# Performance work log

Measured on AMD Instinct MI355X. Metric: run time of the kernel, lower is better.

Reference implementation:

```python
import jax, jax.numpy as jnp
import numpy as np

EPS = 1e-8

def setup_inputs() -> dict:
    key = jax.random.key(0)
    k1, k2, k3, k4 = jax.random.split(key, 4)
    b, in_c, out_c, style_c, k, h, w = 8, 512, 512, 512, 3, 64, 64
    return {
        "input": jax.random.normal(k1, (b, in_c, h, w), dtype=jnp.float32),
        "style": jax.random.normal(k2, (b, style_c), dtype=jnp.float32),
        "w_affine": jax.random.normal(k3, (in_c, style_c), dtype=jnp.float32),  # Linear weight, init N(0,1), runtime-scaled
        "b_affine": jnp.ones((1, in_c), dtype=jnp.float32),                     # Bias init_value=1.0
        "w_conv": jax.random.normal(k4, (out_c, in_c, k, k), dtype=jnp.float32),
    }

def reference(input, style, w_affine, b_affine, w_conv):
    b, in_c, h, w = input.shape
    out_c, _, kh, kw = w_conv.shape
    # Equalized-LR runtime scales (lr_mul=1):
    affine_scale = 1.0 / (w_affine.shape[1] ** 0.5)          # he_std for Linear
    conv_scale = 1.0 / ((in_c * kh * kw) ** 0.5)             # he_std for conv weight
    # affine: Linear + Bias (bias initialized to 1.0)
    s = style @ w_affine.T * affine_scale + b_affine          # [b, in_c]
    # modulate: per-sample weight tensor [b, out_c, in_c, kh, kw]
    wgt = s[:, None, :, None, None] * (w_conv * conv_scale)[None]
    # demodulate
    demod = jax.lax.rsqrt(jnp.sum(wgt * wgt, axis=(2, 3, 4), keepdims=True) + EPS)
    wgt = wgt * demod
    # grouped conv with groups = batch (stride=1, padding=1)
    x = input.reshape(1, b * in_c, h, w)
    wgt = wgt.reshape(b * out_c, in_c, kh, kw)
    out = jax.lax.conv_general_dilated(
        x, wgt,
        window_strides=(1, 1),
        padding=[(1, 1), (1, 1)],
        dimension_numbers=("NCHW", "OIHW", "NCHW"),
        feature_group_count=b,
    )
    return out.reshape(b, out_c, h, w)
```

## Files before the change

### kernel.cpp

```cpp
#include <hip/hip_runtime.h>
#include <hip/hip_bf16.h>

#define BB 8
#define CIN 512
#define COUT 512
#define HH 64
#define WW 64

#define AFF_SCALE 0.044194173824159216f
#define CONV_SCALE 0.014731391274719736f
#define CONV_SCALE2 (1.0f/4608.0f)

typedef short s16x8 __attribute__((ext_vector_type(8)));
typedef float f32x16 __attribute__((ext_vector_type(16)));

__device__ __forceinline__ unsigned short f2bf(float f) {
  __hip_bfloat16 h = __float2bfloat16(f);
  return *reinterpret_cast<unsigned short*>(&h);
}

__device__ __forceinline__ void gload_lds16(const void* g, void* l) {
  __builtin_amdgcn_global_load_lds(
      (const __attribute__((address_space(1))) unsigned int*)g,
      (__attribute__((address_space(3))) unsigned int*)l, 16, 0, 0);
}

__global__ __launch_bounds__(256) void prep1_kernel(
    const float* __restrict__ style, const float* __restrict__ wa,
    const float* __restrict__ ba, float* __restrict__ smod,
    const float* __restrict__ wc, float* __restrict__ wsq,
    ushort* __restrict__ wfrag) {
  int bb = blockIdx.x;
  if (bb < 1024) {
    int wid  = (bb << 2) + (threadIdx.x >> 6);
    int lane = threadIdx.x & 63;
    int b  = wid >> 9;
    int ic = wid & 511;
    const float* s = style + b * CIN;
    const float* w = wa + (size_t)ic * CIN;
    float sum = 0.f;
#pragma unroll
    for (int k = 0; k < CIN / 64; ++k) sum += s[lane + 64 * k] * w[lane + 64 * k];
#pragma unroll
    for (int off = 32; off; off >>= 1) sum += __shfl_down(sum, off, 64);
    if (lane == 0) smod[wid] = sum * AFF_SCALE + ba[ic];
  } else if (bb < 2048) {
    int i = (bb - 1024) * 256 + threadIdx.x;
    const float* p = wc + (size_t)i * 9;
    float s = 0.f;
#pragma unroll
    for (int k = 0; k < 9; ++k) { float v = p[k]; s += v * v; }
    wsq[i] = s;
  } else {
    int n = (bb - 2048) * 256 + threadIdx.x;
    int l    = n & 63;
    int ks   = (n >> 6) & 1;
    int mf   = (n >> 7) & 15;
    int widx = n >> 11;
    int g = widx / 9, p = widx % 9;
    int kh = p % 3, kw = p / 3;
    int oc  = mf * 32 + (l & 31);
    int ic0 = g * 32 + ks * 16 + 8 * (l >> 5);
    s16x8 o;
#pragma unroll
    for (int j = 0; j < 8; ++j) {
      float v = wc[((size_t)oc * CIN + ic0 + j) * 9 + kh * 3 + kw];
      o[j] = (short)f2bf(v);
    }
    *(s16x8*)(wfrag + (size_t)n * 8) = o;
  }
}

__global__ __launch_bounds__(256) void prep2_kernel(
    const float* __restrict__ smod, const float* __restrict__ wsq,
    float* __restrict__ demod,
    const float* __restrict__ xin, ushort* __restrict__ xt) {
  int bb = blockIdx.x;
  if (bb < 1024) {
    int wid  = (bb << 2) + (threadIdx.x >> 6);
    int lane = threadIdx.x & 63;
    int b  = wid >> 9;
    int oc = wid & 511;
    const float* s = smod + b * CIN;
    const float* w = wsq + (size_t)oc * CIN;
    float sum = 0.f;
#pragma unroll
    for (int k = 0; k < CIN / 64; ++k) {
      float sv = s[lane + 64 * k];
      sum += sv * sv * w[lane + 64 * k];
    }
#pragma unroll
    for (int off = 32; off; off >>= 1) sum += __shfl_down(sum, off, 64);
    if (lane == 0) demod[wid] = rsqrtf(sum * CONV_SCALE2 + 1e-8f) * CONV_SCALE;
  } else {
    int n = (bb - 1024) * 256 + threadIdx.x;
    int kg = n & 3;
    int x  = (n >> 2) & 63;
    int y  = (n >> 8) & 63;
    int g  = (n >> 14) & 15;
    int b  = n >> 18;
    int ic0 = g * 32 + kg * 8;
    const float* sp = smod + b * CIN + ic0;
    const float* xp = xin + (((size_t)b * CIN + ic0) * HH + y) * WW + x;
    s16x8 o;
#pragma unroll
    for (int j = 0; j < 8; ++j) {
      float v = xp[(size_t)j * HH * WW] * sp[j];
      o[j] = (short)f2bf(v);
    }
    *(s16x8*)(xt + (size_t)n * 8) = o;
  }
}

#define XS_ROW 4224
#define XS_BUF (6 * XS_ROW)
#define WS_BUFSZ 8192

#define MFMA1(A_, B_, C_) __builtin_amdgcn_mfma_f32_32x32x16_bf16(A_, B_, C_, 0, 0, 0)

#define MHK(KF, SX, SY) \
  __builtin_amdgcn_s_setprio(1); \
  acc[0][0] = MFMA1(wA[KF],     SX[0 + (KF)], acc[0][0]); \
  acc[1][0] = MFMA1(wA[2 + KF], SX[0 + (KF)], acc[1][0]); \
  acc[0][1] = MFMA1(wA[KF],     SX[2 + (KF)], acc[0][1]); \
  acc[1][1] = MFMA1(wA[2 + KF], SX[2 + (KF)], acc[1][1]); \
  acc[0][2] = MFMA1(wA[KF],     SY[0 + (KF)], acc[0][2]); \
  acc[1][2] = MFMA1(wA[2 + KF], SY[0 + (KF)], acc[1][2]); \
  acc[0][3] = MFMA1(wA[KF],     SY[2 + (KF)], acc[0][3]); \
  acc[1][3] = MFMA1(wA[2 + KF], SY[2 + (KF)], acc[1][3]); \
  __builtin_amdgcn_s_setprio(0);

#define LOADSLOT(S, RR, DXI) \
  S[0] = *(const s16x8*)(xs_r + (wr2 + (RR)) * XS_ROW + addrV[0][DXI][0]); \
  S[1] = *(const s16x8*)(xs_r + (wr2 + (RR)) * XS_ROW + addrV[0][DXI][1]); \
  S[2] = *(const s16x8*)(xs_r + (wr2 + (RR)) * XS_ROW + addrV[1][DXI][0]); \
  S[3] = *(const s16x8*)(xs_r + (wr2 + (RR)) * XS_ROW + addrV[1][DXI][1]);

#define ENTRYB2 \
  __builtin_amdgcn_sched_barrier(0); \
  asm volatile("s_waitcnt vmcnt(2) lgkmcnt(0)" ::: "memory"); \
  __builtin_amdgcn_sched_barrier(0); \
  __builtin_amdgcn_s_barrier(); \
  __builtin_amdgcn_sched_barrier(0);

#define ENTRYB8 \
  __builtin_amdgcn_sched_barrier(0); \
  asm volatile("s_waitcnt vmcnt(8) lgkmcnt(0)" ::: "memory"); \
  __builtin_amdgcn_sched_barrier(0); \
  __builtin_amdgcn_s_barrier(); \
  __builtin_amdgcn_sched_barrier(0);

#define ENTRYB0 \
  __builtin_amdgcn_sched_barrier(0); \
  asm volatile("s_waitcnt vmcnt(0) lgkmcnt(0)" ::: "memory"); \
  __builtin_amdgcn_sched_barrier(0); \
  __builtin_amdgcn_s_barrier(); \
  __builtin_amdgcn_sched_barrier(0);

#define AREAD(P) { \
  const char* wsp_ = wsL + ((P) % 3) * WS_BUFSZ + aoff; \
  wA[0] = *(const s16x8*)(wsp_); \
  wA[1] = *(const s16x8*)(wsp_ + 1024); \
  wA[2] = *(const s16x8*)(wsp_ + 2048); \
  wA[3] = *(const s16x8*)(wsp_ + 3072); }

#define WSISSUE(P) { \
  const char* ws_s = wsg + (size_t)((P) + 2) * 32768; \
  char* ws_d = wsdst + (((P) + 2) % 3) * WS_BUFSZ; \
  gload_lds16(ws_s, ws_d); \
  gload_lds16(ws_s + 4096, ws_d + 4096); }

#define GBODY(GG) \
{ \
  const char* xs_r = (const char*)lds + (GG) * XS_BUF; \
  char* xs_w = lds + ((GG) ^ 1) * XS_BUF; \
  const char* wsg = wssrcb + (size_t)(g2 * 18 + (GG) * 9) * 32768; \
   ENTRYB2 AREAD(0) \
         LOADSLOT(bA, 0, 0) LOADSLOT(bB, 1, 0) \
         WSISSUE(0) \
         MHK(0, bA, bB) LOADSLOT(bC, 2, 0) MHK(1, bA, bB) \
   ENTRYB2 AREAD(1) WSISSUE(1) \
         MHK(0, bB, bC) LOADSLOT(bA, 3, 0) MHK(1, bB, bC) \
   ENTRYB2 AREAD(2) WSISSUE(2) \
         MHK(0, bC, bA) LOADSLOT(bB, 0, 1) MHK(1, bC, bA) LOADSLOT(bC, 1, 1) \
   ENTRYB2 AREAD(3) WSISSUE(3) \
         MHK(0, bB, bC) LOADSLOT(bA, 2, 1) MHK(1, bB, bC) \
   ENTRYB2 AREAD(4) WSISSUE(4) \
         MHK(0, bC, bA) LOADSLOT(bB, 3, 1) MHK(1, bC, bA) \
   ENTRYB2 AREAD(5) WSISSUE(5) \
         MHK(0, bA, bB) LOADSLOT(bC, 0, 2) MHK(1, bA, bB) LOADSLOT(bA, 1, 2) \
   ENTRYB2 AREAD(6) WSISSUE(6) \
         stage6(xtb, (size_t)(b * 16 + g2 * 2 + (GG) + 1) * 262144, srcoff, xs_w, trash, lds_woff, y0); \
         MHK(0, bC, bA) LOADSLOT(bB, 2, 2) MHK(1, bC, bA) \
   ENTRYB8 AREAD(7) WSISSUE(7) \
         MHK(0, bA, bB) LOADSLOT(bC, 3, 2) MHK(1, bA, bB) \
   ENTRYB8 AREAD(8) WSISSUE(8) \
         MHK(0, bB, bC) MHK(1, bB, bC) \
}

#define GBODY_LAST \
{ \
  const char* xs_r = (const char*)lds + XS_BUF; \
  const char* wsg = wssrcb + (size_t)(7 * 18 + 9) * 32768; \
   ENTRYB2 AREAD(0) \
         LOADSLOT(bA, 0, 0) LOADSLOT(bB, 1, 0) \
         WSISSUE(0) \
         MHK(0, bA, bB) LOADSLOT(bC, 2, 0) MHK(1, bA, bB) \
   ENTRYB2 AREAD(1) WSISSUE(1) \
         MHK(0, bB, bC) LOADSLOT(bA, 3, 0) MHK(1, bB, bC) \
   ENTRYB2 AREAD(2) WSISSUE(2) \
         MHK(0, bC, bA) LOADSLOT(bB, 0, 1) MHK(1, bC, bA) LOADSLOT(bC, 1, 1) \
   ENTRYB2 AREAD(3) WSISSUE(3) \
         MHK(0, bB, bC) LOADSLOT(bA, 2, 1) MHK(1, bB, bC) \
   ENTRYB2 AREAD(4) WSISSUE(4) \
         MHK(0, bC, bA) LOADSLOT(bB, 3, 1) MHK(1, bC, bA) \
   ENTRYB2 AREAD(5) WSISSUE(5) \
         MHK(0, bA, bB) LOADSLOT(bC, 0, 2) MHK(1, bA, bB) LOADSLOT(bA, 1, 2) \
   ENTRYB2 AREAD(6) WSISSUE(6) \
         MHK(0, bC, bA) LOADSLOT(bB, 2, 2) MHK(1, bC, bA) \
   ENTRYB0 AREAD(7) \
         MHK(0, bA, bB) LOADSLOT(bC, 3, 2) MHK(1, bA, bB) \
   ENTRYB0 AREAD(8) \
         MHK(0, bB, bC) MHK(1, bB, bC) \
}

__device__ __forceinline__ void stage6(const char* xtb, size_t gbase, int srcoff,
                                       char* xs_w, char* trash, int lds_woff, int y0) {
  __builtin_amdgcn_sched_barrier(0);
#pragma unroll
  for (int r = 0; r < 6; ++r) {
    int gy = y0 - 1 + r;
    bool ok = (gy >= 0) && (gy < HH);
    int gyc = ok ? gy : (gy < 0 ? 0 : HH - 1);
    char* dst = ok ? (xs_w + r * XS_ROW + lds_woff) : (trash + lds_woff);
    gload_lds16(xtb + gbase + (size_t)gyc * 4096 + srcoff, dst);
  }
  __builtin_amdgcn_sched_barrier(0);
}

__global__ __launch_bounds__(256, 2) void conv_mfma(
    const ushort* __restrict__ xt,
    const ushort* __restrict__ wfrag,
    const float* __restrict__ demod,
    float* __restrict__ out) {
  __shared__ char lds[2 * XS_BUF + 3 * WS_BUFSZ + XS_ROW];

  int tid = threadIdx.x;
  int l = tid & 63, w = tid >> 6;
  int wm = w >> 1, wr = w & 1;
  int wr2 = wr * 2;
  int bid = blockIdx.x;
  int ocb = bid & 3;
  int b   = (bid >> 2) & 7;
  int yt  = bid >> 5;
  int y0  = yt * 4;

  const char* wsL = (const char*)lds + 2 * XS_BUF;
  char* wsdst = lds + 2 * XS_BUF + tid * 16;
  char* trash = lds + 2 * XS_BUF + 3 * WS_BUFSZ;

  f32x16 acc[2][4];
#pragma unroll
  for (int i = 0; i < 2; ++i)
#pragma unroll
    for (int j = 0; j < 4; ++j)
#pragma unroll
      for (int e = 0; e < 16; ++e) acc[i][j][e] = 0.f;

  if (tid < 96) {
    int buf = tid & 1, side = (tid >> 1) & 1, kgz = (tid >> 2) & 3, r = tid >> 4;
    int chunk = side ? (260 + kgz) : kgz;
    *(int4*)(lds + buf * XS_BUF + r * XS_ROW + chunk * 16) = int4{0, 0, 0, 0};
  }
  if (y0 == 0) {
    for (int i = tid; i < 512; i += 256) {
      int buf = i & 1, chunk = 4 + (i >> 1);
      *(int4*)(lds + buf * XS_BUF + chunk * 16) = int4{0, 0, 0, 0};
    }
  }
  if (y0 == 60) {
    for (int i = tid; i < 512; i += 256) {
      int buf = i & 1, chunk = 4 + (i >> 1);
      *(int4*)(lds + buf * XS_BUF + 5 * XS_ROW + chunk * 16) = int4{0, 0, 0, 0};
    }
  }

  int addrV[2][3][2];
  {
    int lm = l & 31, kh2 = l >> 5;
#pragma unroll
    for (int ph = 0; ph < 2; ++ph)
#pragma unroll
      for (int dxi = 0; dxi < 3; ++dxi)
#pragma unroll
        for (int ks = 0; ks < 2; ++ks) {
          int col = ph * 32 + lm + dxi;
          int kg  = kh2 + 2 * ks;
          addrV[ph][dxi][ks] = (col * 4 + (kg ^ ((col >> 1) & 3))) * 16;
        }
  }

  int col_s = 1 + w * 16 + (l >> 2);
  int srcoff = (col_s - 1) * 64 + ((l & 3) ^ ((col_s >> 1) & 3)) * 16;
  int lds_woff = 64 + w * 1024;

  const char* xtb = (const char*)xt;
  const char* wssrcb = (const char*)wfrag + (size_t)ocb * 8192 + (size_t)tid * 16;
  int aoff = wm * 4096 + l * 16;

  {
    size_t gbase = (size_t)(b * 16) * 262144;
#pragma unroll
    for (int r = 0; r < 6; ++r) {
      int gy = y0 - 1 + r;
      if (gy >= 0 && gy < HH)
        gload_lds16(xtb + gbase + (size_t)gy * 4096 + srcoff,
                    lds + r * XS_ROW + lds_woff);
    }
    gload_lds16(wssrcb,          wsdst);
    gload_lds16(wssrcb + 4096,   wsdst + 4096);
    gload_lds16(wssrcb + 32768,        wsdst + WS_BUFSZ);
    gload_lds16(wssrcb + 32768 + 4096, wsdst + WS_BUFSZ + 4096);
  }
  __syncthreads();

  s16x8 wA[4];
  s16x8 bA[4], bB[4], bC[4];

  for (int g2 = 0; g2 < 7; ++g2) {
    GBODY(0)
    GBODY(1)
  }
  {
    const int g2 = 7;
    GBODY(0)
    GBODY_LAST
  }

  int gy_base = y0 + wr2;
  int colbase = l & 31;
  int rowadd = 4 * (l >> 5);
#pragma unroll
  for (int q = 0; q < 2; ++q) {
#pragma unroll
    for (int reg = 0; reg < 16; ++reg) {
      int row = (reg & 3) + 8 * (reg >> 2) + rowadd;
      int oc = ocb * 128 + (wm * 2 + q) * 32 + row;
      float dm = demod[b * COUT + oc];
#pragma unroll
      for (int n = 0; n < 4; ++n) {
        int gy = gy_base + (n >> 1);
        int px = (n & 1) * 32 + colbase;
        out[((size_t)(b * COUT + oc)) * 4096 + gy * 64 + px] = acc[q][n][reg] * dm;
      }
    }
  }
}

extern "C" void kernel_launch(void* const* d_in, const int* in_sizes, int n_in,
                              void* d_out, int out_size, void* d_ws, size_t ws_size,
                              hipStream_t stream) {
  const float* input = (const float*)d_in[0];
  const float* style = (const float*)d_in[1];
  const float* wa    = (const float*)d_in[2];
  const float* ba    = (const float*)d_in[3];
  const float* wconv = (const float*)d_in[4];
  float* out = (float*)d_out;

  float* smod  = (float*)d_ws;
  float* demod = smod + BB * CIN;
  float* wsq   = demod + BB * COUT;
  ushort* wfrag = (ushort*)(wsq + (size_t)COUT * CIN);
  ushort* xt    = wfrag + (size_t)16 * 9 * 32 * 64 * 8;

  prep1_kernel<<<3200, 256, 0, stream>>>(style, wa, ba, smod, wconv, wsq, wfrag);
  prep2_kernel<<<9216, 256, 0, stream>>>(smod, wsq, demod, input, xt);
  conv_mfma<<<BB * 4 * 16, 256, 0, stream>>>(xt, wfrag, demod, out);
}
```

Before: 146.5 us.

## Widen conv block to 256 output channels with 512 threads and 4-deep weight ring

Each workgroup now has 512 threads and computes 256 output channels instead of 128, which halves the grid. Each staged input row tile is therefore reused across twice as many output channels, and input staging is split three chunks per wave using packed descriptors. The weight-fragment LDS ring grows from three to four buffers, with prefetch issued three steps ahead and A-fragment reads moved to the end of the previous step. In exchange, LDS use grows to roughly 118KB, so likely only one block fits per CU, and the grid becomes a single wave of large blocks.

```diff
diff --git a/kernel.cpp b/kernel.cpp
--- a/kernel.cpp
+++ b/kernel.cpp
@@ -114,7 +114,7 @@
 
 #define XS_ROW 4224
 #define XS_BUF (6 * XS_ROW)
-#define WS_BUFSZ 8192
+#define WS_BUFSZ 16384
 
 #define MFMA1(A_, B_, C_) __builtin_amdgcn_mfma_f32_32x32x16_bf16(A_, B_, C_, 0, 0, 0)
 
@@ -143,121 +143,119 @@
   __builtin_amdgcn_s_barrier(); \
   __builtin_amdgcn_sched_barrier(0);
 
-#define ENTRYB8 \
+#define ENTRYB5 \
   __builtin_amdgcn_sched_barrier(0); \
-  asm volatile("s_waitcnt vmcnt(8) lgkmcnt(0)" ::: "memory"); \
+  asm volatile("s_waitcnt vmcnt(5) lgkmcnt(0)" ::: "memory"); \
   __builtin_amdgcn_sched_barrier(0); \
   __builtin_amdgcn_s_barrier(); \
   __builtin_amdgcn_sched_barrier(0);
 
-#define ENTRYB0 \
-  __builtin_amdgcn_sched_barrier(0); \
-  asm volatile("s_waitcnt vmcnt(0) lgkmcnt(0)" ::: "memory"); \
-  __builtin_amdgcn_sched_barrier(0); \
-  __builtin_amdgcn_s_barrier(); \
-  __builtin_amdgcn_sched_barrier(0);
-
-#define AREAD(P) { \
-  const char* wsp_ = wsL + ((P) % 3) * WS_BUFSZ + aoff; \
+#define AREADB(BUF) { \
+  const char* wsp_ = wsL + (BUF) * WS_BUFSZ + aoff; \
   wA[0] = *(const s16x8*)(wsp_); \
   wA[1] = *(const s16x8*)(wsp_ + 1024); \
   wA[2] = *(const s16x8*)(wsp_ + 2048); \
   wA[3] = *(const s16x8*)(wsp_ + 3072); }
 
-#define WSISSUE(P) { \
-  const char* ws_s = wsg + (size_t)((P) + 2) * 32768; \
-  char* ws_d = wsdst + (((P) + 2) % 3) * WS_BUFSZ; \
-  gload_lds16(ws_s, ws_d); \
-  gload_lds16(ws_s + 4096, ws_d + 4096); }
+#define WSISSUE(GG, P) { \
+  const char* s_ = wsg + (size_t)((P) + 3) * 32768; \
+  char* d_ = wsdst + (((GG) + (P) + 3) & 3) * WS_BUFSZ; \
+  gload_lds16(s_, d_); \
+  gload_lds16(s_ + 8192, d_ + 8192); }
+
+__device__ __forceinline__ void stage3(const char* xtb, size_t gbase,
+                                       const int* sdesc, char* xs_w,
+                                       char* trash, int y0) {
+  __builtin_amdgcn_sched_barrier(0);
+#pragma unroll
+  for (int j = 0; j < 3; ++j) {
+    int d = sdesc[j];
+    int so   = d & 8191;
+    int doff = (d >> 13) & 32767;
+    int r    = d >> 28;
+    int gy = y0 - 1 + r;
+    bool ok = (gy >= 0) && (gy < HH);
+    int gyc = ok ? gy : (gy < 0 ? 0 : HH - 1);
+    char* dst = ok ? (xs_w + doff) : trash;
+    gload_lds16(xtb + gbase + (size_t)gyc * 4096 + so, dst);
+  }
+  __builtin_amdgcn_sched_barrier(0);
+}
 
 #define GBODY(GG) \
 { \
-  const char* xs_r = (const char*)lds + (GG) * XS_BUF; \
-  char* xs_w = lds + ((GG) ^ 1) * XS_BUF; \
-  const char* wsg = wssrcb + (size_t)(g2 * 18 + (GG) * 9) * 32768; \
-   ENTRYB2 AREAD(0) \
+  const char* xs_r = (const char*)lds + ((GG) & 1) * XS_BUF; \
+  char* xs_w = lds + ((((GG) & 1)) ^ 1) * XS_BUF; \
+  const char* wsg = wssrc0 + (size_t)((g4 * 4 + (GG)) * 9) * 32768; \
+   ENTRYB2 \
          LOADSLOT(bA, 0, 0) LOADSLOT(bB, 1, 0) \
-         WSISSUE(0) \
-         MHK(0, bA, bB) LOADSLOT(bC, 2, 0) MHK(1, bA, bB) \
-   ENTRYB2 AREAD(1) WSISSUE(1) \
-         MHK(0, bB, bC) LOADSLOT(bA, 3, 0) MHK(1, bB, bC) \
-   ENTRYB2 AREAD(2) WSISSUE(2) \
-         MHK(0, bC, bA) LOADSLOT(bB, 0, 1) MHK(1, bC, bA) LOADSLOT(bC, 1, 1) \
-   ENTRYB2 AREAD(3) WSISSUE(3) \
-         MHK(0, bB, bC) LOADSLOT(bA, 2, 1) MHK(1, bB, bC) \
-   ENTRYB2 AREAD(4) WSISSUE(4) \
-         MHK(0, bC, bA) LOADSLOT(bB, 3, 1) MHK(1, bC, bA) \
-   ENTRYB2 AREAD(5) WSISSUE(5) \
-         MHK(0, bA, bB) LOADSLOT(bC, 0, 2) MHK(1, bA, bB) LOADSLOT(bA, 1, 2) \
-   ENTRYB2 AREAD(6) WSISSUE(6) \
-         stage6(xtb, (size_t)(b * 16 + g2 * 2 + (GG) + 1) * 262144, srcoff, xs_w, trash, lds_woff, y0); \
-         MHK(0, bC, bA) LOADSLOT(bB, 2, 2) MHK(1, bC, bA) \
-   ENTRYB8 AREAD(7) WSISSUE(7) \
-         MHK(0, bA, bB) LOADSLOT(bC, 3, 2) MHK(1, bA, bB) \
-   ENTRYB8 AREAD(8) WSISSUE(8) \
-         MHK(0, bB, bC) MHK(1, bB, bC) \
+         WSISSUE(GG, 0) \
+         MHK(0, bA, bB) LOADSLOT(bC, 2, 0) MHK(1, bA, bB) AREADB(((GG) + 1) & 3) \
+   ENTRYB2 WSISSUE(GG, 1) \
+         MHK(0, bB, bC) LOADSLOT(bA, 3, 0) MHK(1, bB, bC) AREADB(((GG) + 2) & 3) \
+   ENTRYB2 WSISSUE(GG, 2) \
+         MHK(0, bC, bA) LOADSLOT(bB, 0, 1) MHK(1, bC, bA) LOADSLOT(bC, 1, 1) AREADB(((GG) + 3) & 3) \
+   ENTRYB2 WSISSUE(GG, 3) \
+         MHK(0, bB, bC) LOADSLOT(bA, 2, 1) MHK(1, bB, bC) AREADB(((GG) + 0) & 3) \
+   ENTRYB2 WSISSUE(GG, 4) \
+         MHK(0, bC, bA) LOADSLOT(bB, 3, 1) MHK(1, bC, bA) AREADB(((GG) + 1) & 3) \
+   ENTRYB2 WSISSUE(GG, 5) \
+         MHK(0, bA, bB) LOADSLOT(bC, 0, 2) MHK(1, bA, bB) LOADSLOT(bA, 1, 2) AREADB(((GG) + 2) & 3) \
+   ENTRYB2 WSISSUE(GG, 6) \
+         stage3(xtb, (size_t)(b * 16 + g4 * 4 + (GG) + 1) * 262144, sdesc, xs_w, trash, y0); \
+         MHK(0, bC, bA) LOADSLOT(bB, 2, 2) MHK(1, bC, bA) AREADB(((GG) + 3) & 3) \
+   ENTRYB5 WSISSUE(GG, 7) \
+         MHK(0, bA, bB) LOADSLOT(bC, 3, 2) MHK(1, bA, bB) AREADB(((GG) + 0) & 3) \
+   ENTRYB5 WSISSUE(GG, 8) \
+         MHK(0, bB, bC) MHK(1, bB, bC) AREADB(((GG) + 1) & 3) \
 }
 
 #define GBODY_LAST \
 { \
   const char* xs_r = (const char*)lds + XS_BUF; \
-  const char* wsg = wssrcb + (size_t)(7 * 18 + 9) * 32768; \
-   ENTRYB2 AREAD(0) \
+  const char* wsg = wssrc0 + (size_t)(15 * 9) * 32768; \
+   ENTRYB2 \
          LOADSLOT(bA, 0, 0) LOADSLOT(bB, 1, 0) \
-         WSISSUE(0) \
-         MHK(0, bA, bB) LOADSLOT(bC, 2, 0) MHK(1, bA, bB) \
-   ENTRYB2 AREAD(1) WSISSUE(1) \
-         MHK(0, bB, bC) LOADSLOT(bA, 3, 0) MHK(1, bB, bC) \
-   ENTRYB2 AREAD(2) WSISSUE(2) \
-         MHK(0, bC, bA) LOADSLOT(bB, 0, 1) MHK(1, bC, bA) LOADSLOT(bC, 1, 1) \
-   ENTRYB2 AREAD(3) WSISSUE(3) \
-         MHK(0, bB, bC) LOADSLOT(bA, 2, 1) MHK(1, bB, bC) \
-   ENTRYB2 AREAD(4) WSISSUE(4) \
-         MHK(0, bC, bA) LOADSLOT(bB, 3, 1) MHK(1, bC, bA) \
-   ENTRYB2 AREAD(5) WSISSUE(5) \
-         MHK(0, bA, bB) LOADSLOT(bC, 0, 2) MHK(1, bA, bB) LOADSLOT(bA, 1, 2) \
-   ENTRYB2 AREAD(6) WSISSUE(6) \
-         MHK(0, bC, bA) LOADSLOT(bB, 2, 2) MHK(1, bC, bA) \
-   ENTRYB0 AREAD(7) \
-         MHK(0, bA, bB) LOADSLOT(bC, 3, 2) MHK(1, bA, bB) \
-   ENTRYB0 AREAD(8) \
+         WSISSUE(3, 0) \
+         MHK(0, bA, bB) LOADSLOT(bC, 2, 0) MHK(1, bA, bB) AREADB(0) \
+   ENTRYB2 WSISSUE(3, 1) \
+         MHK(0, bB, bC) LOADSLOT(bA, 3, 0) MHK(1, bB, bC) AREADB(1) \
+   ENTRYB2 WSISSUE(3, 2) \
+         MHK(0, bC, bA) LOADSLOT(bB, 0, 1) MHK(1, bC, bA) LOADSLOT(bC, 1, 1) AREADB(2) \
+   ENTRYB2 WSISSUE(3, 3) \
+         MHK(0, bB, bC) LOADSLOT(bA, 2, 1) MHK(1, bB, bC) AREADB(3) \
+   ENTRYB2 WSISSUE(3, 4) \
+         MHK(0, bC, bA) LOADSLOT(bB, 3, 1) MHK(1, bC, bA) AREADB(0) \
+   ENTRYB2 WSISSUE(3, 5) \
+         MHK(0, bA, bB) LOADSLOT(bC, 0, 2) MHK(1, bA, bB) LOADSLOT(bA, 1, 2) AREADB(1) \
+   ENTRYB2 WSISSUE(3, 6) \
+         MHK(0, bC, bA) LOADSLOT(bB, 2, 2) MHK(1, bC, bA) AREADB(2) \
+   ENTRYB2 \
+         MHK(0, bA, bB) LOADSLOT(bC, 3, 2) MHK(1, bA, bB) AREADB(3) \
+   ENTRYB2 \
          MHK(0, bB, bC) MHK(1, bB, bC) \
 }
 
-__device__ __forceinline__ void stage6(const char* xtb, size_t gbase, int srcoff,
-                                       char* xs_w, char* trash, int lds_woff, int y0) {
-  __builtin_amdgcn_sched_barrier(0);
-#pragma unroll
-  for (int r = 0; r < 6; ++r) {
-    int gy = y0 - 1 + r;
-    bool ok = (gy >= 0) && (gy < HH);
-    int gyc = ok ? gy : (gy < 0 ? 0 : HH - 1);
-    char* dst = ok ? (xs_w + r * XS_ROW + lds_woff) : (trash + lds_woff);
-    gload_lds16(xtb + gbase + (size_t)gyc * 4096 + srcoff, dst);
-  }
-  __builtin_amdgcn_sched_barrier(0);
-}
-
-__global__ __launch_bounds__(256, 2) void conv_mfma(
+__global__ __launch_bounds__(512, 2) void conv_mfma(
     const ushort* __restrict__ xt,
     const ushort* __restrict__ wfrag,
     const float* __restrict__ demod,
     float* __restrict__ out) {
-  __shared__ char lds[2 * XS_BUF + 3 * WS_BUFSZ + XS_ROW];
+  __shared__ char lds[2 * XS_BUF + 4 * WS_BUFSZ + XS_ROW];
 
   int tid = threadIdx.x;
   int l = tid & 63, w = tid >> 6;
   int wm = w >> 1, wr = w & 1;
   int wr2 = wr * 2;
   int bid = blockIdx.x;
-  int ocb = bid & 3;
-  int b   = (bid >> 2) & 7;
-  int yt  = bid >> 5;
+  int ocb = bid & 1;
+  int b   = (bid >> 1) & 7;
+  int yt  = bid >> 4;
   int y0  = yt * 4;
 
   const char* wsL = (const char*)lds + 2 * XS_BUF;
   char* wsdst = lds + 2 * XS_BUF + tid * 16;
-  char* trash = lds + 2 * XS_BUF + 3 * WS_BUFSZ;
+  char* trash = lds + 2 * XS_BUF + 4 * WS_BUFSZ;
 
   f32x16 acc[2][4];
 #pragma unroll
@@ -273,13 +271,13 @@
     *(int4*)(lds + buf * XS_BUF + r * XS_ROW + chunk * 16) = int4{0, 0, 0, 0};
   }
   if (y0 == 0) {
-    for (int i = tid; i < 512; i += 256) {
+    for (int i = tid; i < 512; i += 512) {
       int buf = i & 1, chunk = 4 + (i >> 1);
       *(int4*)(lds + buf * XS_BUF + chunk * 16) = int4{0, 0, 0, 0};
     }
   }
   if (y0 == 60) {
-    for (int i = tid; i < 512; i += 256) {
+    for (int i = tid; i < 512; i += 512) {
       int buf = i & 1, chunk = 4 + (i >> 1);
       *(int4*)(lds + buf * XS_BUF + 5 * XS_ROW + chunk * 16) = int4{0, 0, 0, 0};
     }
@@ -300,40 +298,53 @@
         }
   }
 
-  int col_s = 1 + w * 16 + (l >> 2);
-  int srcoff = (col_s - 1) * 64 + ((l & 3) ^ ((col_s >> 1) & 3)) * 16;
-  int lds_woff = 64 + w * 1024;
+  int sdesc[3];
+#pragma unroll
+  for (int j = 0; j < 3; ++j) {
+    int cid = w * 3 + j;
+    int r = cid >> 2, q = cid & 3;
+    int col_s = 1 + q * 16 + (l >> 2);
+    int so = (col_s - 1) * 64 + ((l & 3) ^ ((col_s >> 1) & 3)) * 16;
+    int doff = r * XS_ROW + 64 + q * 1024;
+    sdesc[j] = (r << 28) | (doff << 13) | so;
+  }
 
   const char* xtb = (const char*)xt;
-  const char* wssrcb = (const char*)wfrag + (size_t)ocb * 8192 + (size_t)tid * 16;
+  const char* wssrc0 = (const char*)wfrag + (size_t)ocb * 16384 + (size_t)tid * 16;
   int aoff = wm * 4096 + l * 16;
 
   {
     size_t gbase = (size_t)(b * 16) * 262144;
 #pragma unroll
-    for (int r = 0; r < 6; ++r) {
+    for (int j = 0; j < 3; ++j) {
+      int d = sdesc[j];
+      int so   = d & 8191;
+      int doff = (d >> 13) & 32767;
+      int r    = d >> 28;
       int gy = y0 - 1 + r;
       if (gy >= 0 && gy < HH)
-        gload_lds16(xtb + gbase + (size_t)gy * 4096 + srcoff,
-                    lds + r * XS_ROW + lds_woff);
-    }
-    gload_lds16(wssrcb,          wsdst);
-    gload_lds16(wssrcb + 4096,   wsdst + 4096);
-    gload_lds16(wssrcb + 32768,        wsdst + WS_BUFSZ);
-    gload_lds16(wssrcb + 32768 + 4096, wsdst + WS_BUFSZ + 4096);
+        gload_lds16(xtb + gbase + (size_t)gy * 4096 + so, lds + doff);
+    }
+#pragma unroll
+    for (int k = 0; k < 3; ++k) {
+      const char* s_ = wssrc0 + (size_t)k * 32768;
+      char* d_ = wsdst + k * WS_BUFSZ;
+      gload_lds16(s_, d_);
+      gload_lds16(s_ + 8192, d_ + 8192);
+    }
   }
   __syncthreads();
 
   s16x8 wA[4];
   s16x8 bA[4], bB[4], bC[4];
-
-  for (int g2 = 0; g2 < 7; ++g2) {
-    GBODY(0)
-    GBODY(1)
+  AREADB(0)
+
+  for (int g4 = 0; g4 < 3; ++g4) {
+    GBODY(0) GBODY(1) GBODY(2) GBODY(3)
   }
   {
-    const int g2 = 7;
-    GBODY(0)
+    const int g4 = 3;
+    GBODY(0) GBODY(1) GBODY(2)
     GBODY_LAST
   }
 
@@ -345,7 +356,7 @@
 #pragma unroll
     for (int reg = 0; reg < 16; ++reg) {
       int row = (reg & 3) + 8 * (reg >> 2) + rowadd;
-      int oc = ocb * 128 + (wm * 2 + q) * 32 + row;
+      int oc = ocb * 256 + (wm * 2 + q) * 32 + row;
       float dm = demod[b * COUT + oc];
 #pragma unroll
       for (int n = 0; n < 4; ++n) {
@@ -375,5 +386,5 @@
 
   prep1_kernel<<<3200, 256, 0, stream>>>(style, wa, ba, smod, wconv, wsq, wfrag);
   prep2_kernel<<<9216, 256, 0, stream>>>(smod, wsq, demod, input, xt);
-  conv_mfma<<<BB * 4 * 16, 256, 0, stream>>>(xt, wfrag, demod, out);
-}
+  conv_mfma<<<2 * BB * 16, 512, 0, stream>>>(xt, wfrag, demod, out);
+}
```

Measured after the change: 153.3 us. 4.6% more time.

## Prefetch next-phase LDS fragments into registers before each barrier

Applied to the files above, without the earlier changes.

Reorders the conv main loop so the weight fragments (AREADB) and the first input slots for the next phase are read from LDS at the end of the current phase, before the barrier, rather than right after it. A prologue loads the first fragments before the loop. The goal is to hide LDS read latency behind the MFMA work of the current phase. In exchange, every barrier now waits on vmcnt(0) instead of allowing 2 or 8 outstanding global-to-LDS loads, so global loads can no longer stay in flight across phases and may stall.

```diff
diff --git a/kernel.cpp b/kernel.cpp
--- a/kernel.cpp
+++ b/kernel.cpp
@@ -136,29 +136,21 @@
   S[2] = *(const s16x8*)(xs_r + (wr2 + (RR)) * XS_ROW + addrV[1][DXI][0]); \
   S[3] = *(const s16x8*)(xs_r + (wr2 + (RR)) * XS_ROW + addrV[1][DXI][1]);
 
-#define ENTRYB2 \
-  __builtin_amdgcn_sched_barrier(0); \
-  asm volatile("s_waitcnt vmcnt(2) lgkmcnt(0)" ::: "memory"); \
-  __builtin_amdgcn_sched_barrier(0); \
-  __builtin_amdgcn_s_barrier(); \
-  __builtin_amdgcn_sched_barrier(0);
-
-#define ENTRYB8 \
-  __builtin_amdgcn_sched_barrier(0); \
-  asm volatile("s_waitcnt vmcnt(8) lgkmcnt(0)" ::: "memory"); \
-  __builtin_amdgcn_sched_barrier(0); \
-  __builtin_amdgcn_s_barrier(); \
-  __builtin_amdgcn_sched_barrier(0);
-
-#define ENTRYB0 \
+#define LOADSLOTW(S, RR, DXI) \
+  S[0] = *(const s16x8*)(xs_w + (wr2 + (RR)) * XS_ROW + addrV[0][DXI][0]); \
+  S[1] = *(const s16x8*)(xs_w + (wr2 + (RR)) * XS_ROW + addrV[0][DXI][1]); \
+  S[2] = *(const s16x8*)(xs_w + (wr2 + (RR)) * XS_ROW + addrV[1][DXI][0]); \
+  S[3] = *(const s16x8*)(xs_w + (wr2 + (RR)) * XS_ROW + addrV[1][DXI][1]);
+
+#define ENTRYB \
   __builtin_amdgcn_sched_barrier(0); \
   asm volatile("s_waitcnt vmcnt(0) lgkmcnt(0)" ::: "memory"); \
   __builtin_amdgcn_sched_barrier(0); \
   __builtin_amdgcn_s_barrier(); \
   __builtin_amdgcn_sched_barrier(0);
 
-#define AREAD(P) { \
-  const char* wsp_ = wsL + ((P) % 3) * WS_BUFSZ + aoff; \
+#define AREADB(BUF) { \
+  const char* wsp_ = wsL + (BUF) * WS_BUFSZ + aoff; \
   wA[0] = *(const s16x8*)(wsp_); \
   wA[1] = *(const s16x8*)(wsp_ + 1024); \
   wA[2] = *(const s16x8*)(wsp_ + 2048); \
@@ -175,52 +167,49 @@
   const char* xs_r = (const char*)lds + (GG) * XS_BUF; \
   char* xs_w = lds + ((GG) ^ 1) * XS_BUF; \
   const char* wsg = wssrcb + (size_t)(g2 * 18 + (GG) * 9) * 32768; \
-   ENTRYB2 AREAD(0) \
-         LOADSLOT(bA, 0, 0) LOADSLOT(bB, 1, 0) \
-         WSISSUE(0) \
-         MHK(0, bA, bB) LOADSLOT(bC, 2, 0) MHK(1, bA, bB) \
-   ENTRYB2 AREAD(1) WSISSUE(1) \
-         MHK(0, bB, bC) LOADSLOT(bA, 3, 0) MHK(1, bB, bC) \
-   ENTRYB2 AREAD(2) WSISSUE(2) \
-         MHK(0, bC, bA) LOADSLOT(bB, 0, 1) MHK(1, bC, bA) LOADSLOT(bC, 1, 1) \
-   ENTRYB2 AREAD(3) WSISSUE(3) \
-         MHK(0, bB, bC) LOADSLOT(bA, 2, 1) MHK(1, bB, bC) \
-   ENTRYB2 AREAD(4) WSISSUE(4) \
-         MHK(0, bC, bA) LOADSLOT(bB, 3, 1) MHK(1, bC, bA) \
-   ENTRYB2 AREAD(5) WSISSUE(5) \
-         MHK(0, bA, bB) LOADSLOT(bC, 0, 2) MHK(1, bA, bB) LOADSLOT(bA, 1, 2) \
-   ENTRYB2 AREAD(6) WSISSUE(6) \
+   ENTRYB WSISSUE(0) \
+         MHK(0, bA, bB) LOADSLOT(bC, 2, 0) MHK(1, bA, bB) AREADB(1) \
+   ENTRYB WSISSUE(1) \
+         MHK(0, bB, bC) LOADSLOT(bA, 3, 0) MHK(1, bB, bC) AREADB(2) \
+   ENTRYB WSISSUE(2) \
+         MHK(0, bC, bA) LOADSLOT(bB, 0, 1) MHK(1, bC, bA) LOADSLOT(bC, 1, 1) AREADB(0) \
+   ENTRYB WSISSUE(3) \
+         MHK(0, bB, bC) LOADSLOT(bA, 2, 1) MHK(1, bB, bC) AREADB(1) \
+   ENTRYB WSISSUE(4) \
+         MHK(0, bC, bA) LOADSLOT(bB, 3, 1) MHK(1, bC, bA) AREADB(2) \
+   ENTRYB WSISSUE(5) \
+         MHK(0, bA, bB) LOADSLOT(bC, 0, 2) MHK(1, bA, bB) LOADSLOT(bA, 1, 2) AREADB(0) \
+   ENTRYB WSISSUE(6) \
          stage6(xtb, (size_t)(b * 16 + g2 * 2 + (GG) + 1) * 262144, srcoff, xs_w, trash, lds_woff, y0); \
-         MHK(0, bC, bA) LOADSLOT(bB, 2, 2) MHK(1, bC, bA) \
-   ENTRYB8 AREAD(7) WSISSUE(7) \
-         MHK(0, bA, bB) LOADSLOT(bC, 3, 2) MHK(1, bA, bB) \
-   ENTRYB8 AREAD(8) WSISSUE(8) \
+         MHK(0, bC, bA) LOADSLOT(bB, 2, 2) MHK(1, bC, bA) AREADB(1) \
+   ENTRYB WSISSUE(7) \
+         MHK(0, bA, bB) LOADSLOT(bC, 3, 2) MHK(1, bA, bB) AREADB(2) \
+   ENTRYB WSISSUE(8) \
          MHK(0, bB, bC) MHK(1, bB, bC) \
+         LOADSLOTW(bA, 0, 0) LOADSLOTW(bB, 1, 0) AREADB(0) \
 }
 
 #define GBODY_LAST \
 { \
   const char* xs_r = (const char*)lds + XS_BUF; \
-  const char* wsg = wssrcb + (size_t)(7 * 18 + 9) * 32768; \
-   ENTRYB2 AREAD(0) \
-         LOADSLOT(bA, 0, 0) LOADSLOT(bB, 1, 0) \
-         WSISSUE(0) \
-         MHK(0, bA, bB) LOADSLOT(bC, 2, 0) MHK(1, bA, bB) \
-   ENTRYB2 AREAD(1) WSISSUE(1) \
-         MHK(0, bB, bC) LOADSLOT(bA, 3, 0) MHK(1, bB, bC) \
-   ENTRYB2 AREAD(2) WSISSUE(2) \
-         MHK(0, bC, bA) LOADSLOT(bB, 0, 1) MHK(1, bC, bA) LOADSLOT(bC, 1, 1) \
-   ENTRYB2 AREAD(3) WSISSUE(3) \
-         MHK(0, bB, bC) LOADSLOT(bA, 2, 1) MHK(1, bB, bC) \
-   ENTRYB2 AREAD(4) WSISSUE(4) \
-         MHK(0, bC, bA) LOADSLOT(bB, 3, 1) MHK(1, bC, bA) \
-   ENTRYB2 AREAD(5) WSISSUE(5) \
-         MHK(0, bA, bB) LOADSLOT(bC, 0, 2) MHK(1, bA, bB) LOADSLOT(bA, 1, 2) \
-   ENTRYB2 AREAD(6) WSISSUE(6) \
-         MHK(0, bC, bA) LOADSLOT(bB, 2, 2) MHK(1, bC, bA) \
-   ENTRYB0 AREAD(7) \
-         MHK(0, bA, bB) LOADSLOT(bC, 3, 2) MHK(1, bA, bB) \
-   ENTRYB0 AREAD(8) \
+  const char* wsg = wssrcb + (size_t)(15 * 9) * 32768; \
+   ENTRYB WSISSUE(0) \
+         MHK(0, bA, bB) LOADSLOT(bC, 2, 0) MHK(1, bA, bB) AREADB(1) \
+   ENTRYB WSISSUE(1) \
+         MHK(0, bB, bC) LOADSLOT(bA, 3, 0) MHK(1, bB, bC) AREADB(2) \
+   ENTRYB WSISSUE(2) \
+         MHK(0, bC, bA) LOADSLOT(bB, 0, 1) MHK(1, bC, bA) LOADSLOT(bC, 1, 1) AREADB(0) \
+   ENTRYB WSISSUE(3) \
+         MHK(0, bB, bC) LOADSLOT(bA, 2, 1) MHK(1, bB, bC) AREADB(1) \
+   ENTRYB WSISSUE(4) \
+         MHK(0, bC, bA) LOADSLOT(bB, 3, 1) MHK(1, bC, bA) AREADB(2) \
+   ENTRYB WSISSUE(5) \
+         MHK(0, bA, bB) LOADSLOT(bC, 0, 2) MHK(1, bA, bB) LOADSLOT(bA, 1, 2) AREADB(0) \
+   ENTRYB WSISSUE(6) \
+         MHK(0, bC, bA) LOADSLOT(bB, 2, 2) MHK(1, bC, bA) AREADB(1) \
+   ENTRYB \
+         MHK(0, bA, bB) LOADSLOT(bC, 3, 2) MHK(1, bA, bB) AREADB(2) \
+   ENTRYB \
          MHK(0, bB, bC) MHK(1, bB, bC) \
 }
 
@@ -327,6 +316,13 @@
   s16x8 wA[4];
   s16x8 bA[4], bB[4], bC[4];
 
+  {
+    const char* xs_r = (const char*)lds;
+    AREADB(0)
+    LOADSLOT(bA, 0, 0)
+    LOADSLOT(bB, 1, 0)
+  }
+
   for (int g2 = 0; g2 < 7; ++g2) {
     GBODY(0)
     GBODY(1)
```

After: 298.2 us. 2.03x slower.
